# Optimization experiments

Hardware: AMD Instinct MI355X
Metric: run time of the kernel (lower is better)

Reference implementation:

```python
import jax, jax.numpy as jnp
import numpy as np

B, S, D, O, E, R, TOP_K = 4, 1024, 1024, 1024, 8, 16, 2
SCALING = 32.0 / 16.0  # lora_alpha / r
NEG_INF = -1e9  # stand-in for float('-inf'); exp underflows to 0 identically after softmax shift


def setup_inputs() -> dict:
    key = jax.random.key(0)
    ks = jax.random.split(key, 6)
    return {
        "x": jax.random.normal(ks[0], (B, S, D), jnp.float32),
        "base_w": jax.random.normal(ks[1], (O, D), jnp.float32) * 0.02,
        "base_b": jnp.zeros((O,), jnp.float32),
        "lora_A": jax.random.normal(ks[2], (E, D, R), jnp.float32) * 0.02,
        "lora_B": jax.random.normal(ks[3], (E, R, O), jnp.float32) * 0.02,
        "router_w": jax.random.normal(ks[4], (E, D), jnp.float32) * 0.02,
        "router_b": jnp.zeros((E,), jnp.float32),
    }


def reference(x, base_w, base_b, lora_A, lora_B, router_w, router_b):
    # base layer: F.linear(x, W, b)
    result = jnp.einsum('bsd,od->bso', x, base_w) + base_b
    # per-expert LoRA: ax = x @ A_e, bax = ax @ B_e
    ax = jnp.einsum('bsd,edr->bser', x, lora_A)        # [B,S,E,R]
    bax = jnp.einsum('bser,ero->bseo', ax, lora_B)     # [B,S,E,O]
    # linear router logits
    logits = jnp.einsum('bsd,ed->bse', x, router_w) + router_b  # [B,S,E]
    # top-k routing: mask logits below the k-th largest to -inf
    kth = jax.lax.top_k(logits, TOP_K)[0][..., -1:]
    masked = jnp.where(logits < kth, NEG_INF, logits)
    expert_weights = jax.nn.softmax(masked, axis=-1)   # [B,S,E]
    # combine experts, scale, add to base output
    return result + SCALING * jnp.einsum('bse,bseo->bso', expert_weights, bax)
```

## Files before the change

### kernel.cpp

```cpp
#include <hip/hip_runtime.h>
#include <cmath>

#define M_TOK 4096
#define KD    1024
#define KEXT  1152
#define NOUT  1024
#define ERDIM 128
#define SCALING 2.0f

typedef short bf16x8 __attribute__((ext_vector_type(8)));
typedef float f32x4  __attribute__((ext_vector_type(4)));

__device__ __forceinline__ ushort f2bf(float f) {
    union { float f; unsigned u; } v; v.f = f;
    unsigned r = v.u + 0x7fffu + ((v.u >> 16) & 1u);
    return (ushort)(r >> 16);
}

typedef const unsigned int __attribute__((address_space(1)))* gas_ptr;
typedef unsigned int __attribute__((address_space(3)))* las_ptr;
__device__ __forceinline__ void gld_lds16(const ushort* g, ushort* l) {
    __builtin_amdgcn_global_load_lds((gas_ptr)g, (las_ptr)l, 16, 0, 0);
}

__global__ __launch_bounds__(256) void prep_router(
    const float* __restrict__ x, const float* __restrict__ rw,
    const float* __restrict__ rb, const float* __restrict__ base_w,
    const float* __restrict__ lora_A, const float* __restrict__ lora_B,
    ushort* __restrict__ Aext, ushort* __restrict__ Bext,
    ushort* __restrict__ LAT, float* __restrict__ wgt)
{
    const int tid = threadIdx.x;
    if (blockIdx.x >= 4096) {
        int i = (blockIdx.x - 4096) * 256 + tid;
        const int NB = NOUT * KEXT;
        if (i < NB) {
            int o = i / KEXT;
            int c = i - o * KEXT;
            float v = (c < KD) ? base_w[(size_t)o * KD + c]
                               : lora_B[(size_t)(c - KD) * NOUT + o];
            Bext[i] = f2bf(v);
        } else {
            int j = i - NB;
            int er = j >> 10, d = j & 1023;
            int e = er >> 4, r = er & 15;
            LAT[j] = f2bf(lora_A[((size_t)e * KD + d) * 16 + r]);
        }
        return;
    }
    const int t = blockIdx.x;
    const float4 xv = ((const float4*)(x + (size_t)t * KD))[tid];

    ushort4 xb;
    xb.x = f2bf(xv.x); xb.y = f2bf(xv.y); xb.z = f2bf(xv.z); xb.w = f2bf(xv.w);
    ((ushort4*)(Aext + (size_t)t * KEXT))[tid] = xb;

    double p[8];
    #pragma unroll
    for (int e = 0; e < 8; e++) {
        const float4 wv = ((const float4*)(rw + (size_t)e * KD))[tid];
        p[e] = (double)(xv.x * wv.x) + (double)(xv.y * wv.y) +
               (double)(xv.z * wv.z) + (double)(xv.w * wv.w);
    }

    const int wave = tid >> 6, lane = tid & 63;
    double q0, q1, q2, q3, r0, r1, s;
    {   const bool b = lane & 1;
        double s0 = b ? p[0] : p[1];
        double s1 = b ? p[2] : p[3];
        double s2 = b ? p[4] : p[5];
        double s3 = b ? p[6] : p[7];
        q0 = (b ? p[1] : p[0]) + __shfl_xor(s0, 1);
        q1 = (b ? p[3] : p[2]) + __shfl_xor(s1, 1);
        q2 = (b ? p[5] : p[4]) + __shfl_xor(s2, 1);
        q3 = (b ? p[7] : p[6]) + __shfl_xor(s3, 1);
    }
    {   const bool b = (lane >> 1) & 1;
        double s0 = b ? q0 : q1;
        double s1 = b ? q2 : q3;
        r0 = (b ? q1 : q0) + __shfl_xor(s0, 2);
        r1 = (b ? q3 : q2) + __shfl_xor(s1, 2);
    }
    {   const bool b = (lane >> 2) & 1;
        double s0 = b ? r0 : r1;
        s = (b ? r1 : r0) + __shfl_xor(s0, 4);
    }
    s += __shfl_xor(s, 8);
    s += __shfl_xor(s, 16);
    s += __shfl_xor(s, 32);

    __shared__ double red[4][8];
    __shared__ float  lg[8];
    if (lane < 8) red[wave][lane] = s;
    __syncthreads();
    if (tid < 8) {
        double sum = red[0][tid] + red[1][tid] + red[2][tid] + red[3][tid]
                   + (double)rb[tid];
        lg[tid] = (float)sum;
    }
    __syncthreads();
    if (tid < 8) {
        float my = lg[tid];
        float m1 = -INFINITY, m2 = -INFINITY;
        #pragma unroll
        for (int i = 0; i < 8; i++) {
            float v = lg[i];
            if (v > m1) { m2 = m1; m1 = v; }
            else if (v > m2) { m2 = v; }
        }
        float denom = 0.f;
        #pragma unroll
        for (int i = 0; i < 8; i++)
            if (lg[i] >= m2) denom += expf(lg[i] - m1);
        float w = (my >= m2) ? expf(my - m1) / denom : 0.f;
        wgt[t * 8 + tid] = SCALING * w;
    }
}

__global__ __launch_bounds__(256) void gemm_main(
    const ushort* __restrict__ A, const ushort* __restrict__ B,
    float* __restrict__ C, const float* __restrict__ bias, int ksteps)
{
    __shared__ __attribute__((aligned(16))) ushort As[2][128 * 64];
    __shared__ __attribute__((aligned(16))) ushort Bs[2][64 * 64];

    const int tid  = threadIdx.x;
    const int wave = tid >> 6;
    const int lane = tid & 63;
    const int m0 = blockIdx.x * 128;
    const int n0 = blockIdx.y * 64;

    const int srow = tid >> 3;
    const int scol = ((tid & 7) ^ (srow & 7)) * 8;
    const ushort* aP = A + (size_t)(m0 + srow) * KEXT + scol;
    const ushort* bP = B + (size_t)(n0 + srow) * KEXT + scol;

    const int wr = wave * 32;
    const int fm = lane & 15;
    const int q  = lane >> 4;
    const int rx = fm & 7;

    f32x4 acc[2][4] = {};

    auto stage = [&](int buf, int kk) {
        ushort* a_d = &As[buf][tid * 8];
        ushort* b_d = &Bs[buf][tid * 8];
        #pragma unroll
        for (int p = 0; p < 4; p++)
            gld_lds16(aP + kk + (size_t)(p * 32) * KEXT, a_d + p * 2048);
        #pragma unroll
        for (int p = 0; p < 2; p++)
            gld_lds16(bP + kk + (size_t)(p * 32) * KEXT, b_d + p * 2048);
    };

    stage(0, 0);

    for (int ks = 0; ks < ksteps; ++ks) {
        __syncthreads();
        if (ks + 1 < ksteps)
            stage((ks + 1) & 1, (ks + 1) * 64);

        const ushort* as = &As[ks & 1][0];
        const ushort* bs = &Bs[ks & 1][0];

        bf16x8 af[2][2], bf[2][4];
        #pragma unroll
        for (int kh = 0; kh < 2; kh++) {
            const int sg = ((kh * 4 + q) ^ rx) * 8;
            #pragma unroll
            for (int i = 0; i < 2; i++)
                af[kh][i] = *(const bf16x8*)&as[(wr + i * 16 + fm) * 64 + sg];
            #pragma unroll
            for (int j = 0; j < 4; j++)
                bf[kh][j] = *(const bf16x8*)&bs[(j * 16 + fm) * 64 + sg];
        }
        #pragma unroll
        for (int kh = 0; kh < 2; kh++)
            #pragma unroll
            for (int mi = 0; mi < 2; mi++)
                #pragma unroll
                for (int ni = 0; ni < 4; ni++)
                    acc[mi][ni] = __builtin_amdgcn_mfma_f32_16x16x32_bf16(
                        af[kh][mi], bf[kh][ni], acc[mi][ni], 0, 0, 0);
    }

    const int rr = q * 4;
    #pragma unroll
    for (int ni = 0; ni < 4; ni++) {
        const int col = n0 + ni * 16 + fm;
        const float bv = bias[col];
        #pragma unroll
        for (int mi = 0; mi < 2; mi++) {
            const int row = m0 + wr + mi * 16 + rr;
            #pragma unroll
            for (int r = 0; r < 4; r++)
                C[(size_t)(row + r) * NOUT + col] = acc[mi][ni][r] + bv;
        }
    }
}

__global__ __launch_bounds__(256) void gemm_ax(
    const ushort* __restrict__ A, int lda,
    const ushort* __restrict__ B, int ldb,
    float* __restrict__ C, int ldc,
    int k_per_z, int zstride, int ksteps)
{
    __shared__ __attribute__((aligned(16))) ushort As[2][64 * 64];
    __shared__ __attribute__((aligned(16))) ushort Bs[2][128 * 64];

    const int tid  = threadIdx.x;
    const int wave = tid >> 6;
    const int lane = tid & 63;
    const int m0 = blockIdx.x * 64;
    const int k0 = blockIdx.z * k_per_z;
    C += (size_t)blockIdx.z * zstride;

    const int srow = tid >> 3;
    const int scol = ((tid & 7) ^ (srow & 7)) * 8;
    const ushort* aP = A + (size_t)(m0 + srow) * lda + k0 + scol;
    const ushort* bP = B + (size_t)(srow) * ldb + k0 + scol;

    const int wr = (wave >> 1) * 32;
    const int wc = (wave & 1) * 64;
    const int fm = lane & 15;
    const int q  = lane >> 4;
    const int rx = fm & 7;

    f32x4 acc[2][4] = {};

    auto stage = [&](int buf, int kk) {
        ushort* a_d = &As[buf][tid * 8];
        ushort* b_d = &Bs[buf][tid * 8];
        #pragma unroll
        for (int p = 0; p < 2; p++)
            gld_lds16(aP + kk + (size_t)(p * 32) * lda, a_d + p * 2048);
        #pragma unroll
        for (int p = 0; p < 4; p++)
            gld_lds16(bP + kk + (size_t)(p * 32) * ldb, b_d + p * 2048);
    };

    stage(0, 0);

    for (int ks = 0; ks < ksteps; ++ks) {
        __syncthreads();
        if (ks + 1 < ksteps)
            stage((ks + 1) & 1, (ks + 1) * 64);

        const ushort* as = &As[ks & 1][0];
        const ushort* bs = &Bs[ks & 1][0];

        bf16x8 af[2][2], bf[2][4];
        #pragma unroll
        for (int kh = 0; kh < 2; kh++) {
            const int sg = ((kh * 4 + q) ^ rx) * 8;
            #pragma unroll
            for (int i = 0; i < 2; i++)
                af[kh][i] = *(const bf16x8*)&as[(wr + i * 16 + fm) * 64 + sg];
            #pragma unroll
            for (int j = 0; j < 4; j++)
                bf[kh][j] = *(const bf16x8*)&bs[(wc + j * 16 + fm) * 64 + sg];
        }
        #pragma unroll
        for (int kh = 0; kh < 2; kh++)
            #pragma unroll
            for (int mi = 0; mi < 2; mi++)
                #pragma unroll
                for (int ni = 0; ni < 4; ni++)
                    acc[mi][ni] = __builtin_amdgcn_mfma_f32_16x16x32_bf16(
                        af[kh][mi], bf[kh][ni], acc[mi][ni], 0, 0, 0);
    }

    const int rr = q * 4;
    #pragma unroll
    for (int ni = 0; ni < 4; ni++) {
        const int col = wc + ni * 16 + fm;
        #pragma unroll
        for (int mi = 0; mi < 2; mi++) {
            const int row = m0 + wr + mi * 16 + rr;
            #pragma unroll
            for (int r = 0; r < 4; r++)
                C[(size_t)(row + r) * ldc + col] = acc[mi][ni][r];
        }
    }
}

__global__ __launch_bounds__(256) void ax_combine(
    const float* __restrict__ part, const float* __restrict__ wgt,
    ushort* __restrict__ Aext)
{
    int i = blockIdx.x * 256 + threadIdx.x;
    const int t = i >> 7, er = i & 127;
    const int SL = M_TOK * ERDIM;
    float s = part[i] + part[i + SL] + part[i + 2 * SL] + part[i + 3 * SL];
    float w = wgt[t * 8 + (er >> 4)];
    Aext[(size_t)t * KEXT + KD + er] = f2bf(s * w);
}

extern "C" void kernel_launch(void* const* d_in, const int* in_sizes, int n_in,
                              void* d_out, int out_size, void* d_ws, size_t ws_size,
                              hipStream_t stream) {
    const float* x        = (const float*)d_in[0];
    const float* base_w   = (const float*)d_in[1];
    const float* base_b   = (const float*)d_in[2];
    const float* lora_A   = (const float*)d_in[3];
    const float* lora_B   = (const float*)d_in[4];
    const float* router_w = (const float*)d_in[5];
    const float* router_b = (const float*)d_in[6];
    float* out = (float*)d_out;

    char* ws = (char*)d_ws;
    ushort* Aext = (ushort*)(ws);
    ushort* Bext = (ushort*)(ws + 9437184);
    ushort* LAT  = (ushort*)(ws + 11796480);
    float*  wgt  = (float*) (ws + 12058624);
    float*  part = (float*) (ws + 12189696);

    prep_router<<<9216, 256, 0, stream>>>(
        x, router_w, router_b, base_w, lora_A, lora_B, Aext, Bext, LAT, wgt);
    gemm_ax<<<dim3(64, 1, 4), 256, 0, stream>>>(
        Aext, KEXT, LAT, KD, part, ERDIM,
        256, M_TOK * ERDIM, 4);
    ax_combine<<<2048, 256, 0, stream>>>(part, wgt, Aext);
    gemm_main<<<dim3(32, 16), 256, 0, stream>>>(
        Aext, Bext, out, base_b, 18);
}
```

Measured before the change: 112.3 us.

## Pre-pack weight operands in MFMA fragment order and load B directly from global

```diff
diff --git a/kernel.cpp b/kernel.cpp
--- a/kernel.cpp
+++ b/kernel.cpp
@@ -16,6 +16,10 @@
     unsigned r = v.u + 0x7fffu + ((v.u >> 16) & 1u);
     return (ushort)(r >> 16);
 }
+__device__ __forceinline__ float b2f(ushort u) {
+    union { unsigned u; float f; } v; v.u = ((unsigned)u) << 16;
+    return v.f;
+}
 
 typedef const unsigned int __attribute__((address_space(1)))* gas_ptr;
 typedef unsigned int __attribute__((address_space(3)))* las_ptr;
@@ -23,12 +27,13 @@
     __builtin_amdgcn_global_load_lds((gas_ptr)g, (las_ptr)l, 16, 0, 0);
 }
 
+
 __global__ __launch_bounds__(256) void prep_router(
     const float* __restrict__ x, const float* __restrict__ rw,
     const float* __restrict__ rb, const float* __restrict__ base_w,
     const float* __restrict__ lora_A, const float* __restrict__ lora_B,
-    ushort* __restrict__ Aext, ushort* __restrict__ Bext,
-    ushort* __restrict__ LAT, float* __restrict__ wgt)
+    ushort* __restrict__ Aext, ushort* __restrict__ Bpack,
+    ushort* __restrict__ LATpack, float* __restrict__ wgt)
 {
     const int tid = threadIdx.x;
     if (blockIdx.x >= 4096) {
@@ -39,12 +44,17 @@
             int c = i - o * KEXT;
             float v = (c < KD) ? base_w[(size_t)o * KD + c]
                                : lora_B[(size_t)(c - KD) * NOUT + o];
-            Bext[i] = f2bf(v);
+            int lane = (o & 15) + ((c >> 3) & 3) * 16;
+            int didx = (((o >> 4) * 36 + (c >> 5)) * 64 + lane) * 8 + (c & 7);
+            Bpack[didx] = f2bf(v);
         } else {
             int j = i - NB;
             int er = j >> 10, d = j & 1023;
             int e = er >> 4, r = er & 15;
-            LAT[j] = f2bf(lora_A[((size_t)e * KD + d) * 16 + r]);
+            float v = lora_A[((size_t)e * KD + d) * 16 + r];
+            int lane = (er & 15) + ((d >> 3) & 3) * 16;
+            int didx = (((er >> 4) * 32 + (d >> 5)) * 64 + lane) * 8 + (d & 7);
+            LATpack[didx] = f2bf(v);
         }
         return;
     }
@@ -118,61 +128,60 @@
 }
 
 __global__ __launch_bounds__(256) void gemm_main(
-    const ushort* __restrict__ A, const ushort* __restrict__ B,
-    float* __restrict__ C, const float* __restrict__ bias, int ksteps)
+    const ushort* __restrict__ A, const ushort* __restrict__ Bp,
+    float* __restrict__ C, const float* __restrict__ bias)
 {
     __shared__ __attribute__((aligned(16))) ushort As[2][128 * 64];
-    __shared__ __attribute__((aligned(16))) ushort Bs[2][64 * 64];
 
     const int tid  = threadIdx.x;
     const int wave = tid >> 6;
     const int lane = tid & 63;
-    const int m0 = blockIdx.x * 128;
-    const int n0 = blockIdx.y * 64;
+    const int m0  = blockIdx.x * 128;
+    const int ntb = blockIdx.y * 4;
 
     const int srow = tid >> 3;
     const int scol = ((tid & 7) ^ (srow & 7)) * 8;
     const ushort* aP = A + (size_t)(m0 + srow) * KEXT + scol;
-    const ushort* bP = B + (size_t)(n0 + srow) * KEXT + scol;
 
     const int wr = wave * 32;
     const int fm = lane & 15;
     const int q  = lane >> 4;
     const int rx = fm & 7;
 
+    const ushort* bBase = Bp + (size_t)lane * 8;
+
     f32x4 acc[2][4] = {};
 
-    auto stage = [&](int buf, int kk) {
-        ushort* a_d = &As[buf][tid * 8];
-        ushort* b_d = &Bs[buf][tid * 8];
+    auto stageA = [&](int buf, int kk) {
+        ushort* d = &As[buf][tid * 8];
         #pragma unroll
         for (int p = 0; p < 4; p++)
-            gld_lds16(aP + kk + (size_t)(p * 32) * KEXT, a_d + p * 2048);
-        #pragma unroll
-        for (int p = 0; p < 2; p++)
-            gld_lds16(bP + kk + (size_t)(p * 32) * KEXT, b_d + p * 2048);
+            gld_lds16(aP + kk + (size_t)(p * 32) * KEXT, d + p * 2048);
     };
 
-    stage(0, 0);
-
-    for (int ks = 0; ks < ksteps; ++ks) {
+    stageA(0, 0);
+
+    for (int ks = 0; ks < 18; ++ks) {
         __syncthreads();
-        if (ks + 1 < ksteps)
-            stage((ks + 1) & 1, (ks + 1) * 64);
+        if (ks + 1 < 18)
+            stageA((ks + 1) & 1, (ks + 1) * 64);
+
+        bf16x8 bf[2][4];
+        #pragma unroll
+        for (int kh = 0; kh < 2; kh++)
+            #pragma unroll
+            for (int ni = 0; ni < 4; ni++)
+                bf[kh][ni] = *(const bf16x8*)(bBase +
+                    (size_t)((ntb + ni) * 36 + ks * 2 + kh) * 512);
 
         const ushort* as = &As[ks & 1][0];
-        const ushort* bs = &Bs[ks & 1][0];
-
-        bf16x8 af[2][2], bf[2][4];
+        bf16x8 af[2][2];
         #pragma unroll
         for (int kh = 0; kh < 2; kh++) {
             const int sg = ((kh * 4 + q) ^ rx) * 8;
             #pragma unroll
             for (int i = 0; i < 2; i++)
                 af[kh][i] = *(const bf16x8*)&as[(wr + i * 16 + fm) * 64 + sg];
-            #pragma unroll
-            for (int j = 0; j < 4; j++)
-                bf[kh][j] = *(const bf16x8*)&bs[(j * 16 + fm) * 64 + sg];
         }
         #pragma unroll
         for (int kh = 0; kh < 2; kh++)
@@ -187,7 +196,7 @@
     const int rr = q * 4;
     #pragma unroll
     for (int ni = 0; ni < 4; ni++) {
-        const int col = n0 + ni * 16 + fm;
+        const int col = (ntb + ni) * 16 + fm;
         const float bv = bias[col];
         #pragma unroll
         for (int mi = 0; mi < 2; mi++) {
@@ -200,25 +209,21 @@
 }
 
 __global__ __launch_bounds__(256) void gemm_ax(
-    const ushort* __restrict__ A, int lda,
-    const ushort* __restrict__ B, int ldb,
-    float* __restrict__ C, int ldc,
-    int k_per_z, int zstride, int ksteps)
+    const ushort* __restrict__ A, const ushort* __restrict__ Lp,
+    ushort* __restrict__ part)
 {
     __shared__ __attribute__((aligned(16))) ushort As[2][64 * 64];
-    __shared__ __attribute__((aligned(16))) ushort Bs[2][128 * 64];
 
     const int tid  = threadIdx.x;
     const int wave = tid >> 6;
     const int lane = tid & 63;
-    const int m0 = blockIdx.x * 64;
-    const int k0 = blockIdx.z * k_per_z;
-    C += (size_t)blockIdx.z * zstride;
+    const int m0  = blockIdx.x * 64;
+    const int kc0 = blockIdx.z * 8;
+    part += (size_t)blockIdx.z * (M_TOK * ERDIM);
 
     const int srow = tid >> 3;
     const int scol = ((tid & 7) ^ (srow & 7)) * 8;
-    const ushort* aP = A + (size_t)(m0 + srow) * lda + k0 + scol;
-    const ushort* bP = B + (size_t)(srow) * ldb + k0 + scol;
+    const ushort* aP = A + (size_t)(m0 + srow) * KEXT + kc0 * 32 + scol;
 
     const int wr = (wave >> 1) * 32;
     const int wc = (wave & 1) * 64;
@@ -226,39 +231,41 @@
     const int q  = lane >> 4;
     const int rx = fm & 7;
 
+    const ushort* lBase = Lp + (size_t)lane * 8;
+    const int ntw = (wave & 1) * 4;
+
     f32x4 acc[2][4] = {};
 
-    auto stage = [&](int buf, int kk) {
-        ushort* a_d = &As[buf][tid * 8];
-        ushort* b_d = &Bs[buf][tid * 8];
+    auto stageA = [&](int buf, int kk) {
+        ushort* d = &As[buf][tid * 8];
         #pragma unroll
         for (int p = 0; p < 2; p++)
-            gld_lds16(aP + kk + (size_t)(p * 32) * lda, a_d + p * 2048);
-        #pragma unroll
-        for (int p = 0; p < 4; p++)
-            gld_lds16(bP + kk + (size_t)(p * 32) * ldb, b_d + p * 2048);
+            gld_lds16(aP + kk + (size_t)(p * 32) * KEXT, d + p * 2048);
     };
 
-    stage(0, 0);
-
-    for (int ks = 0; ks < ksteps; ++ks) {
+    stageA(0, 0);
+
+    for (int ks = 0; ks < 4; ++ks) {
         __syncthreads();
-        if (ks + 1 < ksteps)
-            stage((ks + 1) & 1, (ks + 1) * 64);
+        if (ks + 1 < 4)
+            stageA((ks + 1) & 1, (ks + 1) * 64);
+
+        bf16x8 bf[2][4];
+        #pragma unroll
+        for (int kh = 0; kh < 2; kh++)
+            #pragma unroll
+            for (int ni = 0; ni < 4; ni++)
+                bf[kh][ni] = *(const bf16x8*)(lBase +
+                    (size_t)((ntw + ni) * 32 + kc0 + ks * 2 + kh) * 512);
 
         const ushort* as = &As[ks & 1][0];
-        const ushort* bs = &Bs[ks & 1][0];
-
-        bf16x8 af[2][2], bf[2][4];
+        bf16x8 af[2][2];
         #pragma unroll
         for (int kh = 0; kh < 2; kh++) {
             const int sg = ((kh * 4 + q) ^ rx) * 8;
             #pragma unroll
             for (int i = 0; i < 2; i++)
                 af[kh][i] = *(const bf16x8*)&as[(wr + i * 16 + fm) * 64 + sg];
-            #pragma unroll
-            for (int j = 0; j < 4; j++)
-                bf[kh][j] = *(const bf16x8*)&bs[(wc + j * 16 + fm) * 64 + sg];
         }
         #pragma unroll
         for (int kh = 0; kh < 2; kh++)
@@ -279,21 +286,44 @@
             const int row = m0 + wr + mi * 16 + rr;
             #pragma unroll
             for (int r = 0; r < 4; r++)
-                C[(size_t)(row + r) * ldc + col] = acc[mi][ni][r];
+                part[(size_t)(row + r) * ERDIM + col] = f2bf(acc[mi][ni][r]);
         }
     }
 }
 
 __global__ __launch_bounds__(256) void ax_combine(
-    const float* __restrict__ part, const float* __restrict__ wgt,
+    const ushort* __restrict__ part, const float* __restrict__ wgt,
     ushort* __restrict__ Aext)
 {
-    int i = blockIdx.x * 256 + threadIdx.x;
-    const int t = i >> 7, er = i & 127;
+    int g = blockIdx.x * 256 + threadIdx.x;
+    const int t = g >> 4, gr = g & 15;
+    const int er0 = gr * 8;
     const int SL = M_TOK * ERDIM;
-    float s = part[i] + part[i + SL] + part[i + 2 * SL] + part[i + 3 * SL];
-    float w = wgt[t * 8 + (er >> 4)];
-    Aext[(size_t)t * KEXT + KD + er] = f2bf(s * w);
+    const int base = t * ERDIM + er0;
+
+    ushort4 p0a = *(const ushort4*)(part + base);
+    ushort4 p0b = *(const ushort4*)(part + base + 4);
+    ushort4 p1a = *(const ushort4*)(part + base + SL);
+    ushort4 p1b = *(const ushort4*)(part + base + SL + 4);
+    ushort4 p2a = *(const ushort4*)(part + base + 2 * SL);
+    ushort4 p2b = *(const ushort4*)(part + base + 2 * SL + 4);
+    ushort4 p3a = *(const ushort4*)(part + base + 3 * SL);
+    ushort4 p3b = *(const ushort4*)(part + base + 3 * SL + 4);
+
+    const float w = wgt[t * 8 + (er0 >> 4)];
+    ushort o[8];
+    o[0] = f2bf((b2f(p0a.x) + b2f(p1a.x) + b2f(p2a.x) + b2f(p3a.x)) * w);
+    o[1] = f2bf((b2f(p0a.y) + b2f(p1a.y) + b2f(p2a.y) + b2f(p3a.y)) * w);
+    o[2] = f2bf((b2f(p0a.z) + b2f(p1a.z) + b2f(p2a.z) + b2f(p3a.z)) * w);
+    o[3] = f2bf((b2f(p0a.w) + b2f(p1a.w) + b2f(p2a.w) + b2f(p3a.w)) * w);
+    o[4] = f2bf((b2f(p0b.x) + b2f(p1b.x) + b2f(p2b.x) + b2f(p3b.x)) * w);
+    o[5] = f2bf((b2f(p0b.y) + b2f(p1b.y) + b2f(p2b.y) + b2f(p3b.y)) * w);
+    o[6] = f2bf((b2f(p0b.z) + b2f(p1b.z) + b2f(p2b.z) + b2f(p3b.z)) * w);
+    o[7] = f2bf((b2f(p0b.w) + b2f(p1b.w) + b2f(p2b.w) + b2f(p3b.w)) * w);
+
+    ushort* dst = Aext + (size_t)t * KEXT + KD + er0;
+    ((ushort4*)dst)[0] = *(ushort4*)&o[0];
+    ((ushort4*)dst)[1] = *(ushort4*)&o[4];
 }
 
 extern "C" void kernel_launch(void* const* d_in, const int* in_sizes, int n_in,
@@ -309,18 +339,16 @@
     float* out = (float*)d_out;
 
     char* ws = (char*)d_ws;
-    ushort* Aext = (ushort*)(ws);
-    ushort* Bext = (ushort*)(ws + 9437184);
-    ushort* LAT  = (ushort*)(ws + 11796480);
-    float*  wgt  = (float*) (ws + 12058624);
-    float*  part = (float*) (ws + 12189696);
+    ushort* Aext    = (ushort*)(ws);
+    ushort* Bpack   = (ushort*)(ws + 9437184);
+    ushort* LATpack = (ushort*)(ws + 11796480);
+    float*  wgt     = (float*) (ws + 12058624);
+    ushort* part    = (ushort*)(ws + 12189696);
 
     prep_router<<<9216, 256, 0, stream>>>(
-        x, router_w, router_b, base_w, lora_A, lora_B, Aext, Bext, LAT, wgt);
-    gemm_ax<<<dim3(64, 1, 4), 256, 0, stream>>>(
-        Aext, KEXT, LAT, KD, part, ERDIM,
-        256, M_TOK * ERDIM, 4);
-    ax_combine<<<2048, 256, 0, stream>>>(part, wgt, Aext);
-    gemm_main<<<dim3(32, 16), 256, 0, stream>>>(
-        Aext, Bext, out, base_b, 18);
-}
+        x, router_w, router_b, base_w, lora_A, lora_B,
+        Aext, Bpack, LATpack, wgt);
+    gemm_ax<<<dim3(64, 1, 4), 256, 0, stream>>>(Aext, LATpack, part);
+    ax_combine<<<256, 256, 0, stream>>>(part, wgt, Aext);
+    gemm_main<<<dim3(32, 16), 256, 0, stream>>>(Aext, Bpack, out, base_b);
+}
```

Measured after the change: 125.2 us. 1.11x slower.
